# Optimization experiments

Hardware: AMD Instinct MI355X
Metric: run time of the kernel (lower is better)

Reference implementation:

```python
import jax, jax.numpy as jnp
import numpy as np
from jax import lax

B, S, D, V, MAXLEN = 32, 2048, 1024, 32000, 2048
EPS = jnp.finfo(jnp.float32).eps  # torch RMSNorm default eps=None -> finfo eps


def setup_inputs() -> dict:
    key = jax.random.key(0)
    ks = jax.random.split(key, 10)
    w = lambda k, shape: (jax.random.normal(k, shape, jnp.float32) * 0.02)
    return {
        "x": jax.random.randint(ks[0], (B, S), 0, V),
        "emb": w(ks[1], (V, D)),
        "pos": w(ks[2], (MAXLEN, D)),
        "conv_w": w(ks[3], (3, D, D)),            # HIO layout (k, in, out)
        "conv_b": jnp.zeros((D,), jnp.float32),
        "wg1": w(ks[4], (D, D)), "bg1": jnp.zeros((D,), jnp.float32),
        "wmv": w(ks[5], (2 * D, D)), "bmv": jnp.zeros((D,), jnp.float32),
        "wmg": w(ks[6], (2 * D, D)), "bmg": jnp.zeros((D,), jnp.float32),
        "wrg": w(ks[7], (2 * D, D)), "brg": jnp.zeros((D,), jnp.float32),
        "rms_w": jnp.ones((D,), jnp.float32),
        "wp": w(ks[8], (2 * D, V)), "bp": jnp.zeros((V,), jnp.float32),
    }


def _rmsnorm(v, rms_w):
    ms = jnp.mean(v * v, axis=-1, keepdims=True)
    return v * lax.rsqrt(ms + EPS) * rms_w


def reference(x, emb, pos, conv_w, conv_b, wg1, bg1, wmv, bmv, wmg, bmg,
              wrg, brg, rms_w, wp, bp):
    seq_len = x.shape[1]
    h = emb[x] + pos[:seq_len]                     # [B, S, D]
    # Conv1d(D, D, k=3, padding=1) over the sequence axis
    h = lax.conv_general_dilated(h, conv_w, window_strides=(1,),
                                 padding=((1, 1),),
                                 dimension_numbers=("NHC", "HIO", "NHC")) + conv_b
    nodes = h * jax.nn.sigmoid(h @ wg1 + bg1)      # gated nodes [B, S, D]

    curr = nodes[:, :-1, :]                        # nodes_past [B, S-1, D]
    while curr.shape[1] > 1:                       # log2(S) static levels
        if curr.shape[1] % 2 != 0:
            curr = jnp.concatenate([curr, curr[:, -1:, :]], axis=1)
        left = curr[:, 0::2, :]
        right = curr[:, 1::2, :]
        combined = jnp.concatenate([left, right], axis=-1)   # [B, n/2, 2D]
        val = combined @ wmv + bmv
        gate = jax.nn.sigmoid(combined @ wmg + bmg)
        merged = _rmsnorm(val * gate, rms_w)
        res_gate = jax.nn.sigmoid(combined @ wrg + brg)
        residual = (left + right) * 0.5
        curr = res_gate * merged + (1.0 - res_gate) * residual

    root = curr[:, 0, :]                           # [B, D]
    last = nodes[:, -2, :]                         # last of nodes_past
    context = jnp.concatenate([root, last], axis=-1)  # [B, 2D]
    return context @ wp + bp                       # logits [B, V]
```

## Files before the change

### kernel.cpp

```cpp
#include <hip/hip_runtime.h>
#include <stdint.h>

typedef __bf16 bf16_t;
typedef __attribute__((ext_vector_type(8))) __bf16 bf16x8;
typedef __attribute__((ext_vector_type(4))) __bf16 bf16x4;
typedef __attribute__((ext_vector_type(4))) float f32x4;

#define NB 32
#define NS 2048
#define ND 1024
#define NV 32000
#define SP 2050

__device__ __forceinline__ float sigmoid_(float x) { return 1.0f / (1.0f + __expf(-x)); }

__device__ __forceinline__ void gload_lds16(const void* g, void* lds) {
  __builtin_amdgcn_global_load_lds((const __attribute__((address_space(1))) void*)g,
                                   (__attribute__((address_space(3))) void*)lds, 16, 0, 0);
}


__global__ void zero_pad_k(bf16_t* h0p) {
  int i = blockIdx.x;
  int b = i >> 1;
  size_t row = (size_t)b * SP + ((i & 1) ? (SP - 1) : 0);
  bf16x4 z = {};
  *(bf16x4*)(h0p + row * ND + threadIdx.x * 4) = z;
}

__global__ void embed_k(const int* __restrict__ x, const float* __restrict__ emb,
                        const float* __restrict__ pos, bf16_t* __restrict__ h0p) {
  int bs = blockIdx.x;
  int b = bs >> 11, s = bs & (NS - 1);
  int idx = x[bs];
  const float* e = emb + (size_t)idx * ND;
  const float* p = pos + (size_t)s * ND;
  bf16_t* o = h0p + ((size_t)b * SP + s + 1) * ND;
  int d = threadIdx.x * 4;
  f32x4 ev = *(const f32x4*)(e + d);
  f32x4 pv = *(const f32x4*)(p + d);
  bf16x4 ov;
  ov[0] = (bf16_t)(ev[0] + pv[0]);
  ov[1] = (bf16_t)(ev[1] + pv[1]);
  ov[2] = (bf16_t)(ev[2] + pv[2]);
  ov[3] = (bf16_t)(ev[3] + pv[3]);
  *(bf16x4*)(o + d) = ov;
}

__global__ void conv_transpose_k(const float* __restrict__ in, bf16_t* __restrict__ out,
                                 int R, int C) {
  __shared__ float tile[32][33];
  int tc = blockIdx.x * 32, tr = blockIdx.y * 32;
  int tx = threadIdx.x;
  for (int i = threadIdx.y; i < 32; i += 8)
    tile[i][tx] = in[(size_t)(tr + i) * C + tc + tx];
  __syncthreads();
  for (int i = threadIdx.y; i < 32; i += 8)
    out[(size_t)(tc + i) * R + tr + tx] = (bf16_t)tile[tx][i];
}

__global__ void dup_row_k(bf16_t* nodes) {
  int b = blockIdx.x;
  const bf16_t* src = nodes + ((size_t)b * NS + NS - 2) * ND;
  bf16_t* dst = nodes + ((size_t)b * NS + NS - 1) * ND;
  int d = threadIdx.x * 4;
  *(bf16x4*)(dst + d) = *(const bf16x4*)(src + d);
}

__global__ void concat3_k(const float* __restrict__ a, const float* __restrict__ b,
                          const float* __restrict__ c, float* __restrict__ o) {
  int i = blockIdx.x * 256 + threadIdx.x;
  o[i] = i < 1024 ? a[i] : (i < 2048 ? b[i - 1024] : c[i - 2048]);
}

template <int EPI>
__global__ __launch_bounds__(512, 2) void gemm256(
    const bf16_t* __restrict__ A, const bf16_t* __restrict__ Bt,
    const float* __restrict__ bias, const void* aux, void* Cout,
    int M, int N, int K, int lda, int batchShift, int batchPad,
    int GX, int gpx, int nxg, int ych) {
  const int tid = threadIdx.x;
  const int lane = tid & 63;
  const int wave = tid >> 6;
  int n0, m0;
  if (nxg == 0) {
    n0 = (blockIdx.x % GX) * 256;
    m0 = (blockIdx.x / GX) * 256;
  } else {
    const int id = blockIdx.x;
    const int xcd = id & 7;
    const int jb = id >> 3;
    const int xg = xcd % nxg;
    const int ysub = xcd / nxg;
    n0 = (xg * gpx + (jb % gpx)) * 256;
    m0 = (ysub * ych + (jb / gpx)) * 256;
  }
  const int waveM = wave >> 2, waveN = wave & 3;

  __shared__ __align__(16) bf16_t sA[2][256 * 64];
  __shared__ __align__(16) bf16_t sB[2][256 * 64];

  const int srow = tid >> 3;
  const int sj = tid & 7;
  const bf16_t* pA[4];
  const bf16_t* pB[4];
#pragma unroll
  for (int idx = 0; idx < 4; ++idx) {
    int lr = idx * 64 + srow;
    int sc = sj ^ (lr & 7);
    int gm = m0 + lr;
    if (gm > M - 1) gm = M - 1;
    size_t grow = (size_t)gm + (size_t)(((unsigned)gm) >> batchShift) * batchPad;
    pA[idx] = A + grow * (size_t)lda + sc * 8;
    int gn = n0 + lr;
    if (gn > N - 1) gn = N - 1;
    pB[idx] = Bt + (size_t)gn * K + sc * 8;
  }
  const int ldsrow = wave * 8;

  auto stageAhalf = [&](int buf, int h) {
#pragma unroll
    for (int r = 0; r < 2; ++r) {
      int idx = h * 2 + r;
      gload_lds16(pA[idx], &sA[buf][(size_t)(idx * 64 + ldsrow) * 64]);
      pA[idx] += 64;
    }
  };
  auto stageBhalf = [&](int buf, int h) {
#pragma unroll
    for (int r = 0; r < 2; ++r) {
      int idx = h * 2 + r;
      gload_lds16(pB[idx], &sB[buf][(size_t)(idx * 64 + ldsrow) * 64]);
      pB[idx] += 64;
    }
  };

  const int rlane = lane & 15;
  const int klane = lane >> 4;
  int offA[8][2], offB[4][2];
#pragma unroll
  for (int i = 0; i < 8; ++i) {
    int ra = waveM * 128 + i * 16 + rlane;
#pragma unroll
    for (int ks = 0; ks < 2; ++ks)
      offA[i][ks] = ra * 128 + (((ks * 4 + klane) ^ (ra & 7)) << 4);
  }
#pragma unroll
  for (int j = 0; j < 4; ++j) {
    int rb = waveN * 64 + j * 16 + rlane;
#pragma unroll
    for (int ks = 0; ks < 2; ++ks)
      offB[j][ks] = rb * 128 + (((ks * 4 + klane) ^ (rb & 7)) << 4);
  }

  f32x4 acc[8][4] = {};

  const int nt = K >> 6;
  stageAhalf(0, 0); stageAhalf(0, 1);
  stageBhalf(0, 0); stageBhalf(0, 1);
  stageBhalf(1, 0); stageBhalf(1, 1);
  asm volatile("s_waitcnt vmcnt(4)" ::: "memory");
  __builtin_amdgcn_s_barrier();

  for (int tt = 0; tt < nt; tt += 2) {
#pragma unroll
    for (int u = 0; u < 2; ++u) {
      const int t = tt + u;
      const char* sa = (const char*)&sA[u][0];
      const char* sb = (const char*)&sB[u][0];
      bf16x8 bfr[4][2];
#pragma unroll
      for (int p = 0; p < 4; ++p) {
        if (p == 0) {
#pragma unroll
          for (int j = 0; j < 4; ++j)
#pragma unroll
            for (int ks = 0; ks < 2; ++ks)
              bfr[j][ks] = *(const bf16x8*)(sb + offB[j][ks]);
          asm volatile("" ::: "memory");
        }
        bf16x8 av[2][2];
#pragma unroll
        for (int i = 0; i < 2; ++i)
#pragma unroll
          for (int ks = 0; ks < 2; ++ks)
            av[i][ks] = *(const bf16x8*)(sa + offA[p * 2 + i][ks]);
        if (p == 0) {
          if (t + 1 < nt) stageAhalf(u ^ 1, 0);
        } else if (p == 1) {
          if (t + 1 < nt) stageAhalf(u ^ 1, 1);
        } else if (p == 2) {
          if (t + 2 < nt) stageBhalf(u, 0);
        } else {
          if (t + 2 < nt) stageBhalf(u, 1);
        }
        if (p == 0) asm volatile("s_waitcnt lgkmcnt(8)" ::: "memory");
        __builtin_amdgcn_s_barrier();
        asm volatile("s_waitcnt lgkmcnt(0)" ::: "memory");
        __builtin_amdgcn_s_setprio(1);
#pragma unroll
        for (int ks = 0; ks < 2; ++ks)
#pragma unroll
          for (int i = 0; i < 2; ++i)
#pragma unroll
            for (int j = 0; j < 4; ++j)
              acc[p * 2 + i][j] = __builtin_amdgcn_mfma_f32_16x16x32_bf16(
                  av[i][ks], bfr[j][ks], acc[p * 2 + i][j], 0, 0, 0);
        __builtin_amdgcn_s_setprio(0);
        if (p < 3) {
          __builtin_amdgcn_s_barrier();
        } else {
          if (t + 2 < nt)
            asm volatile("s_waitcnt vmcnt(4)" ::: "memory");
          else
            asm volatile("s_waitcnt vmcnt(0)" ::: "memory");
          __builtin_amdgcn_s_barrier();
        }
      }
    }
  }

  const int colBase = n0 + waveN * 64 + rlane;
#pragma unroll
  for (int i = 0; i < 8; ++i) {
    const int rowBase = m0 + waveM * 128 + i * 16 + klane * 4;
#pragma unroll
    for (int j = 0; j < 4; ++j) {
      const int col = colBase + j * 16;
      const float bv = bias[col];
#pragma unroll
      for (int r = 0; r < 4; ++r) {
        const int row = rowBase + r;
        if (row >= M) continue;
        float v = acc[i][j][r] + bv;
        size_t o = (size_t)row * N + col;
        if constexpr (EPI == 0) {
          ((bf16_t*)Cout)[o] = (bf16_t)v;
        } else if constexpr (EPI == 1) {
          float hh = (float)((const bf16_t*)aux)[o];
          ((bf16_t*)Cout)[o] = (bf16_t)(hh * sigmoid_(v));
        } else {
          ((bf16_t*)Cout)[o] = (bf16_t)(col < 1024 ? v : sigmoid_(v));
        }
      }
    }
  }
}

template <bool ATOMIC>
__global__ __launch_bounds__(256, 2) void gemm128s(
    const bf16_t* __restrict__ A, const bf16_t* __restrict__ Bt,
    const float* __restrict__ bias, float* __restrict__ Cout,
    int M, int kLen, int nxy) {
  const int tid = threadIdx.x;
  const int lane = tid & 63;
  const int wave = tid >> 6;
  const int id = blockIdx.x;
  const int sk = id / nxy;
  const int rb2 = id % nxy;
  const int n0 = (rb2 % 24) * 128;
  const int m0 = (rb2 / 24) * 128;
  const int kOff = sk * kLen;

  const int waveM = wave >> 1, waveN = wave & 1;

  __shared__ __align__(16) bf16_t sA[2][128 * 64];
  __shared__ __align__(16) bf16_t sB[2][128 * 64];

  f32x4 acc[4][4] = {};

  const int srow = wave * 8 + (lane >> 3);
  const int sj = lane & 7;

  auto stage = [&](int buf, int kk0) {
#pragma unroll
    for (int j = 0; j < 4; ++j) {
      int rowT = j * 32 + srow;
      int k8 = sj ^ (rowT & 7);
      int gm = m0 + rowT;
      if (gm > M - 1) gm = M - 1;
      gload_lds16(A + (size_t)gm * 2048 + (kk0 + k8 * 8), &sA[buf][(j * 256 + wave * 64) * 8]);
      int gn = n0 + rowT;
      gload_lds16(Bt + (size_t)gn * 2048 + (kk0 + k8 * 8), &sB[buf][(j * 256 + wave * 64) * 8]);
    }
  };

  stage(0, kOff);
  __syncthreads();

  const int nt = kLen >> 6;
  int cur = 0;
  const int ar = waveM * 64 + (lane & 15);
  const int br = waveN * 64 + (lane & 15);
  const int kb0 = lane >> 4;

  for (int t = 0; t < nt; ++t) {
    if (t + 1 < nt) stage(cur ^ 1, kOff + (t + 1) * 64);

    const bf16_t* sa = sA[cur];
    const bf16_t* sb = sB[cur];
    bf16x8 af[2][4], bfr[2][4];
#pragma unroll
    for (int ks = 0; ks < 2; ++ks) {
      int kb = kb0 + ks * 4;
#pragma unroll
      for (int i = 0; i < 4; ++i) {
        int ra = ar + i * 16;
        af[ks][i] = *(const bf16x8*)&sa[ra * 64 + ((kb ^ (ra & 7)) * 8)];
        int rbq = br + i * 16;
        bfr[ks][i] = *(const bf16x8*)&sb[rbq * 64 + ((kb ^ (rbq & 7)) * 8)];
      }
    }
#pragma unroll
    for (int ks = 0; ks < 2; ++ks)
#pragma unroll
      for (int i = 0; i < 4; ++i)
#pragma unroll
        for (int j = 0; j < 4; ++j)
          acc[i][j] = __builtin_amdgcn_mfma_f32_16x16x32_bf16(af[ks][i], bfr[ks][j], acc[i][j], 0, 0, 0);
    __syncthreads();
    cur ^= 1;
  }

  const int colBase = n0 + waveN * 64 + (lane & 15);
#pragma unroll
  for (int i = 0; i < 4; ++i) {
    const int rowBase = m0 + waveM * 64 + i * 16 + (lane >> 4) * 4;
#pragma unroll
    for (int jj = 0; jj < 4; ++jj) {
      const int col = colBase + jj * 16;
      const float bv = (!ATOMIC || kOff == 0) ? bias[col] : 0.0f;
#pragma unroll
      for (int r = 0; r < 4; ++r) {
        const int row = rowBase + r;
        if (row >= M) continue;
        float v = acc[i][jj][r] + bv;
        size_t o = (size_t)row * 3072 + col;
        if constexpr (ATOMIC)
          atomicAdd(&Cout[o], v);
        else
          Cout[o] = v;
      }
    }
  }
}

__global__ __launch_bounds__(256) void tree_combine_k(
    const bf16_t* __restrict__ fb, const bf16_t* __restrict__ cur,
    const float* __restrict__ rms_w, bf16_t* __restrict__ outb) {
  const int m = blockIdx.x;
  const int t = threadIdx.x;
  const int d = t * 4;
  const bf16_t* row = fb + (size_t)m * 3072;
  bf16x4 vb = *(const bf16x4*)(row + d);
  bf16x4 gb = *(const bf16x4*)(row + 1024 + d);
  bf16x4 rb = *(const bf16x4*)(row + 2048 + d);
  f32x4 vg;
#pragma unroll
  for (int k = 0; k < 4; ++k) vg[k] = (float)vb[k] * (float)gb[k];
  float ss = vg[0] * vg[0] + vg[1] * vg[1] + vg[2] * vg[2] + vg[3] * vg[3];
#pragma unroll
  for (int o = 32; o > 0; o >>= 1) ss += __shfl_xor(ss, o);
  __shared__ float red[4];
  if ((t & 63) == 0) red[t >> 6] = ss;
  __syncthreads();
  float ms = (red[0] + red[1] + red[2] + red[3]) * (1.0f / ND);
  float scale = rsqrtf(ms + 1.1920929e-07f);
  f32x4 w = *(const f32x4*)(rms_w + d);
  const bf16_t* c0 = cur + (size_t)m * 2048;
  bf16x4 lv = *(const bf16x4*)(c0 + d);
  bf16x4 rv = *(const bf16x4*)(c0 + ND + d);
  bf16x4 o4;
#pragma unroll
  for (int k = 0; k < 4; ++k) {
    float merged = vg[k] * scale * w[k];
    float resid = 0.5f * ((float)lv[k] + (float)rv[k]);
    float g = (float)rb[k];
    o4[k] = (bf16_t)(g * merged + (1.0f - g) * resid);
  }
  *(bf16x4*)(outb + (size_t)m * ND + d) = o4;
}

__global__ __launch_bounds__(256) void tree_combine32_k(
    const float* __restrict__ fb, const bf16_t* __restrict__ cur,
    const float* __restrict__ rms_w, bf16_t* __restrict__ outb) {
  const int m = blockIdx.x;
  const int t = threadIdx.x;
  const int d = t * 4;
  const float* row = fb + (size_t)m * 3072;
  f32x4 v = *(const f32x4*)(row + d);
  f32x4 gl = *(const f32x4*)(row + 1024 + d);
  f32x4 rl = *(const f32x4*)(row + 2048 + d);
  f32x4 vg;
#pragma unroll
  for (int k = 0; k < 4; ++k) vg[k] = v[k] * sigmoid_(gl[k]);
  float ss = vg[0] * vg[0] + vg[1] * vg[1] + vg[2] * vg[2] + vg[3] * vg[3];
#pragma unroll
  for (int o = 32; o > 0; o >>= 1) ss += __shfl_xor(ss, o);
  __shared__ float red[4];
  if ((t & 63) == 0) red[t >> 6] = ss;
  __syncthreads();
  float ms = (red[0] + red[1] + red[2] + red[3]) * (1.0f / ND);
  float scale = rsqrtf(ms + 1.1920929e-07f);
  f32x4 w = *(const f32x4*)(rms_w + d);
  const bf16_t* c0 = cur + (size_t)m * 2048;
  bf16x4 lv = *(const bf16x4*)(c0 + d);
  bf16x4 rv = *(const bf16x4*)(c0 + ND + d);
  bf16x4 o4;
#pragma unroll
  for (int k = 0; k < 4; ++k) {
    float merged = vg[k] * scale * w[k];
    float resid = 0.5f * ((float)lv[k] + (float)rv[k]);
    float g = sigmoid_(rl[k]);
    o4[k] = (bf16_t)(g * merged + (1.0f - g) * resid);
  }
  *(bf16x4*)(outb + (size_t)m * ND + d) = o4;
}

__global__ void build_ctx_k(const bf16_t* __restrict__ root, const bf16_t* __restrict__ nodes,
                            bf16_t* __restrict__ ctxb) {
  int b = blockIdx.x, t = threadIdx.x;
  const bf16_t* r = root + (size_t)b * ND;
  const bf16_t* l = nodes + ((size_t)b * NS + NS - 2) * ND;
  int d = t * 4;
  *(bf16x4*)(ctxb + (size_t)b * 2048 + d) = *(const bf16x4*)(r + d);
  *(bf16x4*)(ctxb + (size_t)b * 2048 + ND + d) = *(const bf16x4*)(l + d);
}

__global__ void init_out_k(const float* __restrict__ bp, float* __restrict__ out) {
  int i = blockIdx.x * 256 + threadIdx.x;
  int b = i / NV;
  out[i] = bp[i - b * NV];
}

__global__ __launch_bounds__(256) void proj_gemm_k(
    const bf16_t* __restrict__ ctxb, const bf16_t* __restrict__ wpT,
    float* __restrict__ out) {
  const int lane = threadIdx.x & 63;
  const int wave = threadIdx.x >> 6;
  const int n0 = blockIdx.x * 256 + wave * 64;
  const int kbase = blockIdx.y * 512;
  const int rl = lane & 15, kl = lane >> 4;
  f32x4 acc[2][4] = {};
#pragma unroll 4
  for (int kt = 0; kt < 16; ++kt) {
    const int k0 = kbase + kt * 32 + kl * 8;
    bf16x8 af[2], bfr[4];
#pragma unroll
    for (int i = 0; i < 2; ++i)
      af[i] = *(const bf16x8*)&ctxb[(size_t)(i * 16 + rl) * 2048 + k0];
#pragma unroll
    for (int j = 0; j < 4; ++j)
      bfr[j] = *(const bf16x8*)&wpT[(size_t)(n0 + j * 16 + rl) * 2048 + k0];
#pragma unroll
    for (int i = 0; i < 2; ++i)
#pragma unroll
      for (int j = 0; j < 4; ++j)
        acc[i][j] = __builtin_amdgcn_mfma_f32_16x16x32_bf16(af[i], bfr[j], acc[i][j], 0, 0, 0);
  }
#pragma unroll
  for (int i = 0; i < 2; ++i)
#pragma unroll
    for (int j = 0; j < 4; ++j)
#pragma unroll
      for (int r = 0; r < 4; ++r) {
        int b = i * 16 + kl * 4 + r;
        int v = n0 + j * 16 + rl;
        atomicAdd(&out[(size_t)b * NV + v], acc[i][j][r]);
      }
}

extern "C" void kernel_launch(void* const* d_in, const int* in_sizes, int n_in,
                              void* d_out, int out_size, void* d_ws, size_t ws_size,
                              hipStream_t stream) {
  const int* x = (const int*)d_in[0];
  const float* emb = (const float*)d_in[1];
  const float* pos = (const float*)d_in[2];
  const float* conv_w = (const float*)d_in[3];
  const float* conv_b = (const float*)d_in[4];
  const float* wg1 = (const float*)d_in[5];
  const float* bg1 = (const float*)d_in[6];
  const float* wmv = (const float*)d_in[7];
  const float* bmv = (const float*)d_in[8];
  const float* wmg = (const float*)d_in[9];
  const float* bmg = (const float*)d_in[10];
  const float* wrg = (const float*)d_in[11];
  const float* brg = (const float*)d_in[12];
  const float* rms_w = (const float*)d_in[13];
  const float* wp = (const float*)d_in[14];
  const float* bp = (const float*)d_in[15];
  float* out = (float*)d_out;

  char* ws = (char*)d_ws;
  size_t off = 0;
  auto alloc = [&](size_t bytes) -> void* {
    void* p = ws + off;
    off += (bytes + 255) & ~(size_t)255;
    return p;
  };
  bf16_t* h0p = (bf16_t*)alloc((size_t)NB * SP * ND * 2);
  bf16_t* h = (bf16_t*)alloc((size_t)NB * NS * ND * 2);
  bf16_t* nodes = (bf16_t*)alloc((size_t)NB * NS * ND * 2);
  bf16_t* tb0 = (bf16_t*)alloc((size_t)NB * 1024 * ND * 2);
  bf16_t* tb1 = (bf16_t*)alloc((size_t)NB * 1024 * ND * 2);
  bf16_t* convT = (bf16_t*)alloc((size_t)ND * 3072 * 2);
  bf16_t* wg1T = (bf16_t*)alloc((size_t)ND * 1024 * 2);
  bf16_t* wAllT = (bf16_t*)alloc((size_t)3072 * 2048 * 2);
  float* bAll = (float*)alloc((size_t)3072 * 4);
  bf16_t* ctxb = (bf16_t*)alloc((size_t)NB * 2048 * 2);
  if (off > ws_size) return;
  bf16_t* fbuf = (bf16_t*)ws;
  float* fbuf32 = (float*)ws;
  bf16_t* wpT = (bf16_t*)ws;

  dim3 t256(256), tb32(32, 8);

  conv_transpose_k<<<dim3(ND / 32, 3072 / 32), tb32, 0, stream>>>(conv_w, convT, 3072, ND);
  conv_transpose_k<<<dim3(ND / 32, ND / 32), tb32, 0, stream>>>(wg1, wg1T, ND, ND);
  conv_transpose_k<<<dim3(ND / 32, 2048 / 32), tb32, 0, stream>>>(wmv, wAllT, 2048, ND);
  conv_transpose_k<<<dim3(ND / 32, 2048 / 32), tb32, 0, stream>>>(wmg, wAllT + (size_t)1024 * 2048, 2048, ND);
  conv_transpose_k<<<dim3(ND / 32, 2048 / 32), tb32, 0, stream>>>(wrg, wAllT + (size_t)2048 * 2048, 2048, ND);
  concat3_k<<<12, t256, 0, stream>>>(bmv, bmg, brg, bAll);

  zero_pad_k<<<64, t256, 0, stream>>>(h0p);
  embed_k<<<NB * NS, t256, 0, stream>>>(x, emb, pos, h0p);

  gemm256<0><<<1024, 512, 0, stream>>>(h0p, convT, conv_b, nullptr, h,
                                       NB * NS, ND, 3072, ND, 11, 2, 4, 1, 4, 128);
  gemm256<1><<<1024, 512, 0, stream>>>(h, wg1T, bg1, h, nodes,
                                       NB * NS, ND, ND, ND, 0, 0, 4, 1, 4, 128);
  dup_row_k<<<NB, t256, 0, stream>>>(nodes);

  const bf16_t* cur = nodes;
  bf16_t* bufs[2] = {tb0, tb1};
  int pp = 0;
  for (int L = NS; L > 1; L >>= 1) {
    int M = NB * (L / 2);
    if (M >= 16384) {
      int GY = M / 256;
      gemm256<3><<<12 * GY, 512, 0, stream>>>(cur, wAllT, bAll, nullptr, fbuf,
                                              M, 3072, 2048, 2048, 0, 0, 12, 3, 4, GY / 2);
      tree_combine_k<<<M, t256, 0, stream>>>(fbuf, cur, rms_w, bufs[pp]);
    } else {
      int GY = (M + 127) / 128;
      int nxy = 24 * GY;
      int SK = 1;
      while (nxy * SK < 768 && SK < 16) SK <<= 1;
      if (SK > 1) {
        hipMemsetAsync(fbuf32, 0, (size_t)M * 3072 * 4, stream);
        gemm128s<true><<<nxy * SK, t256, 0, stream>>>(cur, wAllT, bAll, fbuf32,
                                                      M, 2048 / SK, nxy);
      } else {
        gemm128s<false><<<nxy, t256, 0, stream>>>(cur, wAllT, bAll, fbuf32, M, 2048, nxy);
      }
      tree_combine32_k<<<M, t256, 0, stream>>>(fbuf32, cur, rms_w, bufs[pp]);
    }
    cur = bufs[pp];
    pp ^= 1;
  }

  build_ctx_k<<<NB, t256, 0, stream>>>(cur, nodes, ctxb);
  conv_transpose_k<<<dim3(NV / 32, 2048 / 32), tb32, 0, stream>>>(wp, wpT, 2048, NV);
  init_out_k<<<NB * NV / 256, t256, 0, stream>>>(bp, out);
  proj_gemm_k<<<dim3(NV / 256, 4), t256, 0, stream>>>(ctxb, wpT, out);
}
```

Baseline: 2.332 ms.

## Fuse small tree levels into one persistent kernel with grid barriers

```diff
diff --git a/kernel.cpp b/kernel.cpp
--- a/kernel.cpp
+++ b/kernel.cpp
@@ -247,104 +247,6 @@
   }
 }
 
-template <bool ATOMIC>
-__global__ __launch_bounds__(256, 2) void gemm128s(
-    const bf16_t* __restrict__ A, const bf16_t* __restrict__ Bt,
-    const float* __restrict__ bias, float* __restrict__ Cout,
-    int M, int kLen, int nxy) {
-  const int tid = threadIdx.x;
-  const int lane = tid & 63;
-  const int wave = tid >> 6;
-  const int id = blockIdx.x;
-  const int sk = id / nxy;
-  const int rb2 = id % nxy;
-  const int n0 = (rb2 % 24) * 128;
-  const int m0 = (rb2 / 24) * 128;
-  const int kOff = sk * kLen;
-
-  const int waveM = wave >> 1, waveN = wave & 1;
-
-  __shared__ __align__(16) bf16_t sA[2][128 * 64];
-  __shared__ __align__(16) bf16_t sB[2][128 * 64];
-
-  f32x4 acc[4][4] = {};
-
-  const int srow = wave * 8 + (lane >> 3);
-  const int sj = lane & 7;
-
-  auto stage = [&](int buf, int kk0) {
-#pragma unroll
-    for (int j = 0; j < 4; ++j) {
-      int rowT = j * 32 + srow;
-      int k8 = sj ^ (rowT & 7);
-      int gm = m0 + rowT;
-      if (gm > M - 1) gm = M - 1;
-      gload_lds16(A + (size_t)gm * 2048 + (kk0 + k8 * 8), &sA[buf][(j * 256 + wave * 64) * 8]);
-      int gn = n0 + rowT;
-      gload_lds16(Bt + (size_t)gn * 2048 + (kk0 + k8 * 8), &sB[buf][(j * 256 + wave * 64) * 8]);
-    }
-  };
-
-  stage(0, kOff);
-  __syncthreads();
-
-  const int nt = kLen >> 6;
-  int cur = 0;
-  const int ar = waveM * 64 + (lane & 15);
-  const int br = waveN * 64 + (lane & 15);
-  const int kb0 = lane >> 4;
-
-  for (int t = 0; t < nt; ++t) {
-    if (t + 1 < nt) stage(cur ^ 1, kOff + (t + 1) * 64);
-
-    const bf16_t* sa = sA[cur];
-    const bf16_t* sb = sB[cur];
-    bf16x8 af[2][4], bfr[2][4];
-#pragma unroll
-    for (int ks = 0; ks < 2; ++ks) {
-      int kb = kb0 + ks * 4;
-#pragma unroll
-      for (int i = 0; i < 4; ++i) {
-        int ra = ar + i * 16;
-        af[ks][i] = *(const bf16x8*)&sa[ra * 64 + ((kb ^ (ra & 7)) * 8)];
-        int rbq = br + i * 16;
-        bfr[ks][i] = *(const bf16x8*)&sb[rbq * 64 + ((kb ^ (rbq & 7)) * 8)];
-      }
-    }
-#pragma unroll
-    for (int ks = 0; ks < 2; ++ks)
-#pragma unroll
-      for (int i = 0; i < 4; ++i)
-#pragma unroll
-        for (int j = 0; j < 4; ++j)
-          acc[i][j] = __builtin_amdgcn_mfma_f32_16x16x32_bf16(af[ks][i], bfr[ks][j], acc[i][j], 0, 0, 0);
-    __syncthreads();
-    cur ^= 1;
-  }
-
-  const int colBase = n0 + waveN * 64 + (lane & 15);
-#pragma unroll
-  for (int i = 0; i < 4; ++i) {
-    const int rowBase = m0 + waveM * 64 + i * 16 + (lane >> 4) * 4;
-#pragma unroll
-    for (int jj = 0; jj < 4; ++jj) {
-      const int col = colBase + jj * 16;
-      const float bv = (!ATOMIC || kOff == 0) ? bias[col] : 0.0f;
-#pragma unroll
-      for (int r = 0; r < 4; ++r) {
-        const int row = rowBase + r;
-        if (row >= M) continue;
-        float v = acc[i][jj][r] + bv;
-        size_t o = (size_t)row * 3072 + col;
-        if constexpr (ATOMIC)
-          atomicAdd(&Cout[o], v);
-        else
-          Cout[o] = v;
-      }
-    }
-  }
-}
-
 __global__ __launch_bounds__(256) void tree_combine_k(
     const bf16_t* __restrict__ fb, const bf16_t* __restrict__ cur,
     const float* __restrict__ rms_w, bf16_t* __restrict__ outb) {
@@ -381,40 +283,160 @@
   *(bf16x4*)(outb + (size_t)m * ND + d) = o4;
 }
 
-__global__ __launch_bounds__(256) void tree_combine32_k(
-    const float* __restrict__ fb, const bf16_t* __restrict__ cur,
-    const float* __restrict__ rms_w, bf16_t* __restrict__ outb) {
-  const int m = blockIdx.x;
-  const int t = threadIdx.x;
-  const int d = t * 4;
-  const float* row = fb + (size_t)m * 3072;
-  f32x4 v = *(const f32x4*)(row + d);
-  f32x4 gl = *(const f32x4*)(row + 1024 + d);
-  f32x4 rl = *(const f32x4*)(row + 2048 + d);
-  f32x4 vg;
-#pragma unroll
-  for (int k = 0; k < 4; ++k) vg[k] = v[k] * sigmoid_(gl[k]);
-  float ss = vg[0] * vg[0] + vg[1] * vg[1] + vg[2] * vg[2] + vg[3] * vg[3];
-#pragma unroll
-  for (int o = 32; o > 0; o >>= 1) ss += __shfl_xor(ss, o);
-  __shared__ float red[4];
-  if ((t & 63) == 0) red[t >> 6] = ss;
+__device__ __forceinline__ void gridbar_(int* cnt) {
+  __threadfence();
   __syncthreads();
-  float ms = (red[0] + red[1] + red[2] + red[3]) * (1.0f / ND);
-  float scale = rsqrtf(ms + 1.1920929e-07f);
-  f32x4 w = *(const f32x4*)(rms_w + d);
-  const bf16_t* c0 = cur + (size_t)m * 2048;
-  bf16x4 lv = *(const bf16x4*)(c0 + d);
-  bf16x4 rv = *(const bf16x4*)(c0 + ND + d);
-  bf16x4 o4;
-#pragma unroll
-  for (int k = 0; k < 4; ++k) {
-    float merged = vg[k] * scale * w[k];
-    float resid = 0.5f * ((float)lv[k] + (float)rv[k]);
-    float g = sigmoid_(rl[k]);
-    o4[k] = (bf16_t)(g * merged + (1.0f - g) * resid);
-  }
-  *(bf16x4*)(outb + (size_t)m * ND + d) = o4;
+  if (threadIdx.x == 0) {
+    __hip_atomic_fetch_add(cnt, 1, __ATOMIC_ACQ_REL, __HIP_MEMORY_SCOPE_AGENT);
+    while (__hip_atomic_load(cnt, __ATOMIC_ACQUIRE, __HIP_MEMORY_SCOPE_AGENT) < 512) {
+      __builtin_amdgcn_s_sleep(1);
+    }
+  }
+  __syncthreads();
+}
+
+__global__ __launch_bounds__(256, 2) void tree_tail_k(
+    const bf16_t* __restrict__ curIn, bf16_t* __restrict__ tbA, bf16_t* __restrict__ tbB,
+    const bf16_t* __restrict__ wAllT, const float* __restrict__ bAll,
+    const float* __restrict__ rms_w, float* __restrict__ fb, int* __restrict__ bar) {
+  __shared__ __align__(16) bf16_t sA[2][128 * 64];
+  __shared__ __align__(16) bf16_t sB[2][128 * 64];
+  const int tid = threadIdx.x;
+  const int lane = tid & 63;
+  const int wave = tid >> 6;
+  const int waveM = wave >> 1, waveN = wave & 1;
+  const int srow = wave * 8 + (lane >> 3);
+  const int sj = lane & 7;
+  const int ar = waveM * 64 + (lane & 15);
+  const int br = waveN * 64 + (lane & 15);
+  const int kb0 = lane >> 4;
+
+  const bf16_t* cur = curIn;
+  bf16_t* outs[2] = {tbA, tbB};
+  int po = 0, barIdx = 0;
+
+  for (int M = 2048; M >= 32; M >>= 1) {
+    const int GY = (M + 127) >> 7;
+    const int nxy = 24 * GY;
+    int SK = 1;
+    while (nxy * SK < 384 && SK < 16) SK <<= 1;
+    const int kLen = 2048 / SK;
+    const bool atom = SK > 1;
+
+    for (int tg = blockIdx.x; tg < nxy * SK; tg += 512) {
+      const int sk = tg / nxy;
+      const int rb2 = tg % nxy;
+      const int n0 = (rb2 % 24) * 128;
+      const int m0 = (rb2 / 24) * 128;
+      const int kOff = sk * kLen;
+      f32x4 acc[4][4] = {};
+      auto stage = [&](int buf, int kk0) {
+#pragma unroll
+        for (int j = 0; j < 4; ++j) {
+          int rowT = j * 32 + srow;
+          int k8 = sj ^ (rowT & 7);
+          int gm = m0 + rowT;
+          if (gm > M - 1) gm = M - 1;
+          gload_lds16(cur + (size_t)gm * 2048 + (kk0 + k8 * 8), &sA[buf][(j * 256 + wave * 64) * 8]);
+          int gn = n0 + rowT;
+          gload_lds16(wAllT + (size_t)gn * 2048 + (kk0 + k8 * 8), &sB[buf][(j * 256 + wave * 64) * 8]);
+        }
+      };
+      stage(0, kOff);
+      __syncthreads();
+      const int nt = kLen >> 6;
+      int cb = 0;
+      for (int t = 0; t < nt; ++t) {
+        if (t + 1 < nt) stage(cb ^ 1, kOff + (t + 1) * 64);
+        const bf16_t* sa = sA[cb];
+        const bf16_t* sb = sB[cb];
+        bf16x8 af[2][4], bfr[2][4];
+#pragma unroll
+        for (int ks = 0; ks < 2; ++ks) {
+          int kb = kb0 + ks * 4;
+#pragma unroll
+          for (int i = 0; i < 4; ++i) {
+            int ra = ar + i * 16;
+            af[ks][i] = *(const bf16x8*)&sa[ra * 64 + ((kb ^ (ra & 7)) * 8)];
+            int rbq = br + i * 16;
+            bfr[ks][i] = *(const bf16x8*)&sb[rbq * 64 + ((kb ^ (rbq & 7)) * 8)];
+          }
+        }
+#pragma unroll
+        for (int ks = 0; ks < 2; ++ks)
+#pragma unroll
+          for (int i = 0; i < 4; ++i)
+#pragma unroll
+            for (int j = 0; j < 4; ++j)
+              acc[i][j] = __builtin_amdgcn_mfma_f32_16x16x32_bf16(af[ks][i], bfr[ks][j], acc[i][j], 0, 0, 0);
+        __syncthreads();
+        cb ^= 1;
+      }
+      const int colBase = n0 + waveN * 64 + (lane & 15);
+#pragma unroll
+      for (int i = 0; i < 4; ++i) {
+        const int rowBase = m0 + waveM * 64 + i * 16 + (lane >> 4) * 4;
+#pragma unroll
+        for (int jj = 0; jj < 4; ++jj) {
+          const int col = colBase + jj * 16;
+          const float bv = (!atom || kOff == 0) ? bAll[col] : 0.0f;
+#pragma unroll
+          for (int r = 0; r < 4; ++r) {
+            const int row = rowBase + r;
+            if (row >= M) continue;
+            float v = acc[i][jj][r] + bv;
+            size_t o = (size_t)row * 3072 + col;
+            if (atom)
+              atomicAdd(&fb[o], v);
+            else
+              fb[o] = v;
+          }
+        }
+      }
+    }
+    gridbar_(bar + barIdx); ++barIdx;
+
+    bf16_t* outb = outs[po];
+    float* red = (float*)sA;
+    for (int m = blockIdx.x; m < M; m += 512) {
+      const float* row = fb + (size_t)m * 3072;
+      const int d = tid * 4;
+      f32x4 v = *(const f32x4*)(row + d);
+      f32x4 gl = *(const f32x4*)(row + 1024 + d);
+      f32x4 rl = *(const f32x4*)(row + 2048 + d);
+      f32x4 vg;
+#pragma unroll
+      for (int k = 0; k < 4; ++k) vg[k] = v[k] * sigmoid_(gl[k]);
+      float ss = vg[0] * vg[0] + vg[1] * vg[1] + vg[2] * vg[2] + vg[3] * vg[3];
+#pragma unroll
+      for (int o = 32; o > 0; o >>= 1) ss += __shfl_xor(ss, o);
+      if ((tid & 63) == 0) red[tid >> 6] = ss;
+      __syncthreads();
+      float ms = (red[0] + red[1] + red[2] + red[3]) * (1.0f / ND);
+      float scale = rsqrtf(ms + 1.1920929e-07f);
+      f32x4 w = *(const f32x4*)(rms_w + d);
+      const bf16_t* c0 = cur + (size_t)m * 2048;
+      bf16x4 lv = *(const bf16x4*)(c0 + d);
+      bf16x4 rv = *(const bf16x4*)(c0 + ND + d);
+      bf16x4 o4;
+#pragma unroll
+      for (int k = 0; k < 4; ++k) {
+        float merged = vg[k] * scale * w[k];
+        float resid = 0.5f * ((float)lv[k] + (float)rv[k]);
+        float g = sigmoid_(rl[k]);
+        o4[k] = (bf16_t)(g * merged + (1.0f - g) * resid);
+      }
+      *(bf16x4*)(outb + (size_t)m * ND + d) = o4;
+      f32x4 z = {};
+      *(f32x4*)((float*)row + d) = z;
+      *(f32x4*)((float*)row + 1024 + d) = z;
+      *(f32x4*)((float*)row + 2048 + d) = z;
+      __syncthreads();
+    }
+    gridbar_(bar + barIdx); ++barIdx;
+    cur = outb;
+    po ^= 1;
+  }
 }
 
 __global__ void build_ctx_k(const bf16_t* __restrict__ root, const bf16_t* __restrict__ nodes,
@@ -508,6 +530,7 @@
   bf16_t* wAllT = (bf16_t*)alloc((size_t)3072 * 2048 * 2);
   float* bAll = (float*)alloc((size_t)3072 * 4);
   bf16_t* ctxb = (bf16_t*)alloc((size_t)NB * 2048 * 2);
+  int* bar = (int*)alloc(256);
   if (off > ws_size) return;
   bf16_t* fbuf = (bf16_t*)ws;
   float* fbuf32 = (float*)ws;
@@ -534,32 +557,22 @@
   const bf16_t* cur = nodes;
   bf16_t* bufs[2] = {tb0, tb1};
   int pp = 0;
-  for (int L = NS; L > 1; L >>= 1) {
+  for (int L = NS; L >= 256; L >>= 1) {
     int M = NB * (L / 2);
-    if (M >= 16384) {
-      int GY = M / 256;
-      gemm256<3><<<12 * GY, 512, 0, stream>>>(cur, wAllT, bAll, nullptr, fbuf,
-                                              M, 3072, 2048, 2048, 0, 0, 12, 3, 4, GY / 2);
-      tree_combine_k<<<M, t256, 0, stream>>>(fbuf, cur, rms_w, bufs[pp]);
-    } else {
-      int GY = (M + 127) / 128;
-      int nxy = 24 * GY;
-      int SK = 1;
-      while (nxy * SK < 768 && SK < 16) SK <<= 1;
-      if (SK > 1) {
-        hipMemsetAsync(fbuf32, 0, (size_t)M * 3072 * 4, stream);
-        gemm128s<true><<<nxy * SK, t256, 0, stream>>>(cur, wAllT, bAll, fbuf32,
-                                                      M, 2048 / SK, nxy);
-      } else {
-        gemm128s<false><<<nxy, t256, 0, stream>>>(cur, wAllT, bAll, fbuf32, M, 2048, nxy);
-      }
-      tree_combine32_k<<<M, t256, 0, stream>>>(fbuf32, cur, rms_w, bufs[pp]);
-    }
+    int GY = M / 256;
+    gemm256<3><<<12 * GY, 512, 0, stream>>>(cur, wAllT, bAll, nullptr, fbuf,
+                                            M, 3072, 2048, 2048, 0, 0, 12, 3, 4, GY / 2);
+    tree_combine_k<<<M, t256, 0, stream>>>(fbuf, cur, rms_w, bufs[pp]);
     cur = bufs[pp];
     pp ^= 1;
   }
 
-  build_ctx_k<<<NB, t256, 0, stream>>>(cur, nodes, ctxb);
+  hipMemsetAsync(bar, 0, 256, stream);
+  tree_tail_k<<<512, t256, 0, stream>>>(cur, bufs[pp], bufs[pp ^ 1], wAllT, bAll,
+                                        rms_w, fbuf32, bar);
+  const bf16_t* root = bufs[pp];
+
+  build_ctx_k<<<NB, t256, 0, stream>>>(root, nodes, ctxb);
   conv_transpose_k<<<dim3(NV / 32, 2048 / 32), tb32, 0, stream>>>(wp, wpT, 2048, NV);
   init_out_k<<<NB * NV / 256, t256, 0, stream>>>(bp, out);
   proj_gemm_k<<<dim3(NV / 256, 4), t256, 0, stream>>>(ctxb, wpT, out);
```

Result: slower. 3.795 ms (+62.7%).

## Replace transposed bf16 MFMA projection with direct fp32 projection kernel

Applied to the files above, without the earlier changes.

```diff
diff --git a/kernel.cpp b/kernel.cpp
--- a/kernel.cpp
+++ b/kernel.cpp
@@ -418,13 +418,16 @@
 }
 
 __global__ void build_ctx_k(const bf16_t* __restrict__ root, const bf16_t* __restrict__ nodes,
-                            bf16_t* __restrict__ ctxb) {
+                            float* __restrict__ ctx) {
   int b = blockIdx.x, t = threadIdx.x;
   const bf16_t* r = root + (size_t)b * ND;
   const bf16_t* l = nodes + ((size_t)b * NS + NS - 2) * ND;
   int d = t * 4;
-  *(bf16x4*)(ctxb + (size_t)b * 2048 + d) = *(const bf16x4*)(r + d);
-  *(bf16x4*)(ctxb + (size_t)b * 2048 + ND + d) = *(const bf16x4*)(l + d);
+#pragma unroll
+  for (int k = 0; k < 4; ++k) {
+    ctx[(size_t)b * 2048 + d + k] = (float)r[d + k];
+    ctx[(size_t)b * 2048 + ND + d + k] = (float)l[d + k];
+  }
 }
 
 __global__ void init_out_k(const float* __restrict__ bp, float* __restrict__ out) {
@@ -433,41 +436,27 @@
   out[i] = bp[i - b * NV];
 }
 
-__global__ __launch_bounds__(256) void proj_gemm_k(
-    const bf16_t* __restrict__ ctxb, const bf16_t* __restrict__ wpT,
+__global__ __launch_bounds__(256) void final_proj_k(
+    const float* __restrict__ ctx, const float* __restrict__ wp,
     float* __restrict__ out) {
-  const int lane = threadIdx.x & 63;
-  const int wave = threadIdx.x >> 6;
-  const int n0 = blockIdx.x * 256 + wave * 64;
-  const int kbase = blockIdx.y * 512;
-  const int rl = lane & 15, kl = lane >> 4;
-  f32x4 acc[2][4] = {};
-#pragma unroll 4
-  for (int kt = 0; kt < 16; ++kt) {
-    const int k0 = kbase + kt * 32 + kl * 8;
-    bf16x8 af[2], bfr[4];
-#pragma unroll
-    for (int i = 0; i < 2; ++i)
-      af[i] = *(const bf16x8*)&ctxb[(size_t)(i * 16 + rl) * 2048 + k0];
-#pragma unroll
-    for (int j = 0; j < 4; ++j)
-      bfr[j] = *(const bf16x8*)&wpT[(size_t)(n0 + j * 16 + rl) * 2048 + k0];
-#pragma unroll
-    for (int i = 0; i < 2; ++i)
-#pragma unroll
-      for (int j = 0; j < 4; ++j)
-        acc[i][j] = __builtin_amdgcn_mfma_f32_16x16x32_bf16(af[i], bfr[j], acc[i][j], 0, 0, 0);
-  }
-#pragma unroll
-  for (int i = 0; i < 2; ++i)
-#pragma unroll
-    for (int j = 0; j < 4; ++j)
-#pragma unroll
-      for (int r = 0; r < 4; ++r) {
-        int b = i * 16 + kl * 4 + r;
-        int v = n0 + j * 16 + rl;
-        atomicAdd(&out[(size_t)b * NV + v], acc[i][j][r]);
-      }
+  const int v = blockIdx.x * 256 + threadIdx.x;
+  const int k0 = blockIdx.y * 256;
+  float acc[NB];
+#pragma unroll
+  for (int b = 0; b < NB; ++b) acc[b] = 0.f;
+  __shared__ float sctx[NB][256];
+  for (int i = threadIdx.x; i < NB * 256; i += 256) {
+    int bb = i >> 8, kk = i & 255;
+    sctx[bb][kk] = ctx[(size_t)bb * 2048 + k0 + kk];
+  }
+  __syncthreads();
+  for (int kk = 0; kk < 256; ++kk) {
+    float wv = wp[(size_t)(k0 + kk) * NV + v];
+#pragma unroll
+    for (int b = 0; b < NB; ++b) acc[b] += sctx[b][kk] * wv;
+  }
+#pragma unroll
+  for (int b = 0; b < NB; ++b) atomicAdd(&out[(size_t)b * NV + v], acc[b]);
 }
 
 extern "C" void kernel_launch(void* const* d_in, const int* in_sizes, int n_in,
@@ -507,11 +496,10 @@
   bf16_t* wg1T = (bf16_t*)alloc((size_t)ND * 1024 * 2);
   bf16_t* wAllT = (bf16_t*)alloc((size_t)3072 * 2048 * 2);
   float* bAll = (float*)alloc((size_t)3072 * 4);
-  bf16_t* ctxb = (bf16_t*)alloc((size_t)NB * 2048 * 2);
+  float* ctx = (float*)alloc((size_t)NB * 2048 * 4);
   if (off > ws_size) return;
   bf16_t* fbuf = (bf16_t*)ws;
   float* fbuf32 = (float*)ws;
-  bf16_t* wpT = (bf16_t*)ws;
 
   dim3 t256(256), tb32(32, 8);
 
@@ -559,8 +547,7 @@
     pp ^= 1;
   }
 
-  build_ctx_k<<<NB, t256, 0, stream>>>(cur, nodes, ctxb);
-  conv_transpose_k<<<dim3(NV / 32, 2048 / 32), tb32, 0, stream>>>(wp, wpT, 2048, NV);
+  build_ctx_k<<<NB, t256, 0, stream>>>(cur, nodes, ctx);
   init_out_k<<<NB * NV / 256, t256, 0, stream>>>(bp, out);
-  proj_gemm_k<<<dim3(NV / 256, 4), t256, 0, stream>>>(ctxb, wpT, out);
-}
+  final_proj_k<<<dim3(NV / 256, 8), t256, 0, stream>>>(ctx, wp, out);
+}
```

Measured after the change: 2.323 ms. Within noise of the previous version (-0.4%).
